# Kernel tuning notes

Measured on AMD Instinct MI355X. Metric: run time of the kernel, lower is better.

The kernel has to match this reference:

```python
import jax, jax.numpy as jnp
import numpy as np

S, D, H, L, FF = 4096, 128, 4, 3, 1024
DH = D // H
LN_EPS = 1e-5


def _layernorm(x, g, b):
    m = jnp.mean(x, axis=-1, keepdims=True)
    v = jnp.mean((x - m) ** 2, axis=-1, keepdims=True)
    return (x - m) * jax.lax.rsqrt(v + LN_EPS) * g + b


def setup_inputs() -> dict:
    key = jax.random.key(0)
    ks = jax.random.split(key, 16)
    w = lambda k, shp, s=0.05: jax.random.normal(k, shp, dtype=jnp.float32) * s
    return {
        "src": jax.random.normal(ks[0], (S, 1, D), dtype=jnp.float32),
        # per-layer transformer params, stacked on leading L axis
        "Wqkv": w(ks[1], (L, 3 * D, D)),
        "bqkv": jnp.zeros((L, 3 * D), jnp.float32),
        "Wo": w(ks[2], (L, D, D)),
        "bo": jnp.zeros((L, D), jnp.float32),
        "ln1_g": jnp.ones((L, D), jnp.float32),
        "ln1_b": jnp.zeros((L, D), jnp.float32),
        "W1": w(ks[3], (L, FF, D)),
        "b1": jnp.zeros((L, FF), jnp.float32),
        "W2": w(ks[4], (L, D, FF)),
        "b2": jnp.zeros((L, D), jnp.float32),
        "ln2_g": jnp.ones((L, D), jnp.float32),
        "ln2_b": jnp.zeros((L, D), jnp.float32),
        "fc1_W": w(ks[5], (D, D)),
        "fc1_b": jnp.zeros((D,), jnp.float32),
        "fc2_W": w(ks[6], (D, D)),
        "fc2_b": jnp.zeros((D,), jnp.float32),
    }


def reference(src, Wqkv, bqkv, Wo, bo, ln1_g, ln1_b, W1, b1, W2, b2,
              ln2_g, ln2_b, fc1_W, fc1_b, fc2_W, fc2_b):
    x = src[:, 0, :]  # [S, D] (batch=1, squeezed as in the torch module)
    scale = 1.0 / np.sqrt(DH).astype(np.float32)
    for l in range(L):  # small fixed layer count
        # --- self-attention (post-norm, as in torch TransformerEncoderLayer, eval mode) ---
        qkv = x @ Wqkv[l].T + bqkv[l]                      # [S, 3D]
        q, k, v = jnp.split(qkv, 3, axis=-1)
        q = q.reshape(S, H, DH)
        k = k.reshape(S, H, DH)
        v = v.reshape(S, H, DH)
        att = jax.nn.softmax(jnp.einsum('shd,thd->hst', q, k) * scale, axis=-1)
        o = jnp.einsum('hst,thd->shd', att, v).reshape(S, D)
        o = o @ Wo[l].T + bo[l]
        x = _layernorm(x + o, ln1_g[l], ln1_b[l])
        # --- feed-forward ---
        f = jax.nn.relu(x @ W1[l].T + b1[l]) @ W2[l].T + b2[l]
        x = _layernorm(x + f, ln2_g[l], ln2_b[l])
    # head
    x = jax.nn.relu(x @ fc1_W.T + fc1_b)
    x = x @ fc2_W.T + fc2_b
    # pairwise cosine similarity, clamped at min 1e-6 (vectorized form of pCosineSim)
    xn = x / jnp.linalg.norm(x, axis=1, keepdims=True)
    return jnp.maximum(xn @ xn.T, 1e-6)
```

## Files before the change

kernel.cpp:

```cpp
#include <hip/hip_runtime.h>
#include <math.h>

#define S 4096
#define QK_SCALE 0.17677669529663687f
#define LOG2E    1.44269504088896f
#define SPLIT 8
#define KS (S / SPLIT)

typedef _Float16 f16x8 __attribute__((ext_vector_type(8)));
typedef _Float16 f16x4 __attribute__((ext_vector_type(4)));
typedef _Float16 f16x2 __attribute__((ext_vector_type(2)));
typedef float f32x4 __attribute__((ext_vector_type(4)));


template<int ROWS>
__device__ __forceinline__ void stageGL(_Float16 (*dst)[128], const _Float16* src,
                                        int ld, int row0, int col0, int tid) {
    int w = tid >> 6, l = tid & 63;
    constexpr int NISS = ROWS / 16;
#pragma unroll
    for (int v = 0; v < NISS; v++) {
        int G = (w * NISS + v) * 64 + l;
        int row = G >> 4, g = G & 15;
        int gs = g ^ (row & 15);
        const void* gp = src + (size_t)(row0 + row) * ld + col0 + gs * 8;
        void* lp = (char*)&dst[0][0] + (size_t)G * 16;
        __builtin_amdgcn_global_load_lds(
            (const __attribute__((address_space(1))) void*)gp,
            (__attribute__((address_space(3))) void*)lp, 16, 0, 0);
    }
}

__device__ __forceinline__ f16x8 rdS(const _Float16 (*B)[128], int row, int qg) {
    return *(const f16x8*)&B[row][(qg ^ (row & 15)) << 3];
}
__device__ __forceinline__ void wrS(_Float16 (*B)[128], int row, int col, _Float16 v) {
    B[row][((((col >> 3) ^ (row & 15))) << 3) | (col & 7)] = v;
}

__global__ __launch_bounds__(256) void setup_cvt(const float* __restrict__ q,
                                                 const float* __restrict__ wo,
                                                 const float* __restrict__ w1,
                                                 const float* __restrict__ w2,
                                                 const float* __restrict__ f1,
                                                 const float* __restrict__ f2,
                                                 _Float16* __restrict__ dst,
                                                 const float* __restrict__ a,
                                                 float* __restrict__ x,
                                                 _Float16* __restrict__ xh)
{
    int bb = blockIdx.x;
    if (bb < 992) {
        const float* src; size_t dof; int lb;
        if (bb < 144)      { src = q;  dof = 0;      lb = bb; }
        else if (bb < 192) { src = wo; dof = 147456; lb = bb - 144; }
        else if (bb < 576) { src = w1; dof = 196608; lb = bb - 192; }
        else if (bb < 960) { src = w2; dof = 589824; lb = bb - 576; }
        else if (bb < 976) { src = f1; dof = 983040; lb = bb - 960; }
        else               { src = f2; dof = 999424; lb = bb - 976; }
        int i = lb * 1024 + threadIdx.x * 4;
        float4 v = *(const float4*)(src + i);
        f16x4 h = {(_Float16)v.x, (_Float16)v.y, (_Float16)v.z, (_Float16)v.w};
        *(f16x4*)(dst + dof + i) = h;
    } else {
        int i = (bb - 992) * 256 + threadIdx.x;
        float4 v = ((const float4*)a)[i];
        ((float4*)x)[i] = v;
        f16x4 h = {(_Float16)v.x, (_Float16)v.y, (_Float16)v.z, (_Float16)v.w};
        ((f16x4*)xh)[i] = h;
    }
}

__global__ __launch_bounds__(256) void gemm_qkv(const _Float16* __restrict__ xh,
                                                const _Float16* __restrict__ Wh,
                                                const float* __restrict__ bias,
                                                _Float16* __restrict__ qh,
                                                _Float16* __restrict__ kh,
                                                _Float16* __restrict__ vt)
{
    __shared__ _Float16 Ah[16][128], Bh[128][128];
    int tid = threadIdx.x, w = tid >> 6, l = tid & 63, lc = l & 15, lr = l >> 4;
    int m0 = blockIdx.x * 16, by = blockIdx.y;

    stageGL<16>(Ah, xh, 128, m0, 0, tid);
    stageGL<128>(Bh, Wh, 128, by * 128, 0, tid);
    __syncthreads();

    f32x4 acc[2];
#pragma unroll
    for (int j = 0; j < 2; j++) acc[j] = {0.f, 0.f, 0.f, 0.f};
#pragma unroll
    for (int ks = 0; ks < 4; ks++) {
        f16x8 af = rdS(Ah, lc, ks * 4 + lr);
#pragma unroll
        for (int j = 0; j < 2; j++) {
            f16x8 bf = rdS(Bh, w * 32 + j * 16 + lc, ks * 4 + lr);
            acc[j] = __builtin_amdgcn_mfma_f32_16x16x32_f16(af, bf, acc[j], 0, 0, 0);
        }
    }

    int mb = m0 + lr * 4;
#pragma unroll
    for (int j = 0; j < 2; j++) {
        int n = w * 32 + j * 16 + lc;
        float bb = bias[by * 128 + n];
        if (by == 0) {
#pragma unroll
            for (int r = 0; r < 4; r++)
                qh[(size_t)(mb + r) * 128 + n] =
                    (_Float16)((acc[j][r] + bb) * (QK_SCALE * LOG2E));
        } else if (by == 1) {
            int hh = n >> 5, d = n & 31;
#pragma unroll
            for (int r = 0; r < 4; r++)
                kh[((size_t)hh * S + mb + r) * 32 + d] = (_Float16)(acc[j][r] + bb);
        } else {
            f16x4 pk;
#pragma unroll
            for (int r = 0; r < 4; r++) pk[r] = (_Float16)(acc[j][r] + bb);
            *(f16x4*)&vt[(size_t)n * S + mb] = pk;
        }
    }
}

__global__ __launch_bounds__(256) void attn_mfma(const _Float16* __restrict__ qh,
                                                 const _Float16* __restrict__ kh,
                                                 const _Float16* __restrict__ vt,
                                                 _Float16* __restrict__ part,
                                                 float* __restrict__ mll)
{
    __shared__ _Float16 Ks[2][64][32];
    __shared__ _Float16 Vt[2][32][72];
    __shared__ _Float16 Ps[4][16][72];
    int h = blockIdx.y, q0 = blockIdx.x * 64, z = blockIdx.z;
    int tid = threadIdx.x;
    int w = tid >> 6, l = tid & 63;
    int lc = l & 15, lr = l >> 4;

    f16x8 qf = *(const f16x8*)&qh[(size_t)(q0 + w * 16 + lc) * 128 + h * 32 + lr * 8];

    const _Float16* khh = kh + (size_t)h * S * 32;
    const _Float16* vth = vt + (size_t)h * 32 * S;

    int krow = tid >> 2, kcol = (tid & 3) * 8;
    int vrow = tid >> 3, vcol = (tid & 7) * 8;

    f32x4 o0 = {0.f, 0.f, 0.f, 0.f}, o1 = {0.f, 0.f, 0.f, 0.f};
    float lp = 0.f;

    int k0 = z * KS;
    {
        f16x8 kr = *(const f16x8*)&khh[(size_t)(k0 + krow) * 32 + kcol];
        f16x8 vr = *(const f16x8*)&vth[(size_t)vrow * S + k0 + vcol];
        *(f16x8*)&Ks[0][krow][kcol] = kr;
        *(f16x8*)&Vt[0][vrow][vcol] = vr;
    }
    __syncthreads();

    int cur = 0;
#pragma unroll 1
    for (int t8 = 0; t8 < KS / 64; t8++) {
        bool more = (t8 + 1 < KS / 64);
        f16x8 kr, vr;
        if (more) {
            int kn = k0 + (t8 + 1) * 64;
            kr = *(const f16x8*)&khh[(size_t)(kn + krow) * 32 + kcol];
            vr = *(const f16x8*)&vth[(size_t)vrow * S + kn + vcol];
        }

        f32x4 st[4];
#pragma unroll
        for (int t = 0; t < 4; t++) {
            f16x8 kf = *(const f16x8*)&Ks[cur][t * 16 + lc][lr * 8];
            f32x4 zz = {0.f, 0.f, 0.f, 0.f};
            st[t] = __builtin_amdgcn_mfma_f32_16x16x32_f16(kf, qf, zz, 0, 0, 0);
        }
#pragma unroll
        for (int t = 0; t < 4; t++) {
            float p0 = exp2f(st[t][0]), p1 = exp2f(st[t][1]);
            float p2 = exp2f(st[t][2]), p3 = exp2f(st[t][3]);
            lp += (p0 + p1) + (p2 + p3);
            f16x2 h0 = {(_Float16)p0, (_Float16)p1};
            f16x2 h1 = {(_Float16)p2, (_Float16)p3};
            *(f16x2*)&Ps[w][lc][t * 16 + lr * 4]     = h0;
            *(f16x2*)&Ps[w][lc][t * 16 + lr * 4 + 2] = h1;
        }
        asm volatile("s_waitcnt lgkmcnt(0)" ::: "memory");
#pragma unroll
        for (int ch = 0; ch < 2; ch++) {
            f16x8 pf = *(const f16x8*)&Ps[w][lc][ch * 32 + lr * 8];
            f16x8 v0 = *(const f16x8*)&Vt[cur][lc][ch * 32 + lr * 8];
            f16x8 v1 = *(const f16x8*)&Vt[cur][16 + lc][ch * 32 + lr * 8];
            o0 = __builtin_amdgcn_mfma_f32_16x16x32_f16(pf, v0, o0, 0, 0, 0);
            o1 = __builtin_amdgcn_mfma_f32_16x16x32_f16(pf, v1, o1, 0, 0, 0);
        }
        if (more) {
            *(f16x8*)&Ks[cur ^ 1][krow][kcol] = kr;
            *(f16x8*)&Vt[cur ^ 1][vrow][vcol] = vr;
            __syncthreads();
        }
        cur ^= 1;
    }

    lp += __shfl_xor(lp, 16);
    lp += __shfl_xor(lp, 32);

    _Float16* pz = part + (size_t)z * 524288;
#pragma unroll
    for (int i = 0; i < 4; i++) {
        int q = q0 + w * 16 + lr * 4 + i;
        pz[(size_t)q * 128 + h * 32 + lc]      = (_Float16)o0[i];
        pz[(size_t)q * 128 + h * 32 + 16 + lc] = (_Float16)o1[i];
    }
    if (l < 16) mll[((size_t)z * 4 + h) * 4096 + q0 + w * 16 + lc] = lp;
}

__global__ __launch_bounds__(256) void wo_ln_merge(const _Float16* __restrict__ part,
                                                   const float* __restrict__ mll,
                                                   const _Float16* __restrict__ Wh,
                                                   const float* __restrict__ bias,
                                                   float* __restrict__ x,
                                                   _Float16* __restrict__ xh,
                                                   const float* __restrict__ g,
                                                   const float* __restrict__ b)
{
    __shared__ _Float16 Ah[16][128], Bh[128][128];
    __shared__ float Red[16][4][2];
    int tid = threadIdx.x, w = tid >> 6, l = tid & 63, lc = l & 15, lr = l >> 4;
    int m0 = blockIdx.x * 16;

    stageGL<128>(Bh, Wh, 128, 0, 0, tid);
    {
        int row = tid >> 4, qg = tid & 15;
        int col0 = qg * 8;
        int q = m0 + row, hh = col0 >> 5;
        float lsum = 0.f;
#pragma unroll
        for (int s = 0; s < SPLIT; s++) lsum += mll[((size_t)s * 4 + hh) * 4096 + q];
        float am[8];
#pragma unroll
        for (int e = 0; e < 8; e++) am[e] = 0.f;
#pragma unroll
        for (int s = 0; s < SPLIT; s++) {
            f16x8 t = *(const f16x8*)&part[(size_t)s * 524288 + (size_t)q * 128 + col0];
#pragma unroll
            for (int e = 0; e < 8; e++) am[e] += (float)t[e];
        }
        float inv = 1.f / lsum;
        f16x8 hv;
#pragma unroll
        for (int e = 0; e < 8; e++) hv[e] = (_Float16)(am[e] * inv);
        *(f16x8*)&Ah[row][(qg ^ (row & 15)) << 3] = hv;
    }
    __syncthreads();

    f32x4 acc[2];
#pragma unroll
    for (int j = 0; j < 2; j++) acc[j] = {0.f, 0.f, 0.f, 0.f};
#pragma unroll
    for (int ks = 0; ks < 4; ks++) {
        f16x8 af = rdS(Ah, lc, ks * 4 + lr);
#pragma unroll
        for (int j = 0; j < 2; j++) {
            f16x8 bf = rdS(Bh, w * 32 + j * 16 + lc, ks * 4 + lr);
            acc[j] = __builtin_amdgcn_mfma_f32_16x16x32_f16(af, bf, acc[j], 0, 0, 0);
        }
    }

#pragma unroll
    for (int j = 0; j < 2; j++) {
        int n = w * 32 + j * 16 + lc;
        float bb = bias[n];
#pragma unroll
        for (int r = 0; r < 4; r++)
            acc[j][r] += bb + x[(size_t)(m0 + lr * 4 + r) * 128 + n];
    }
#pragma unroll
    for (int r = 0; r < 4; r++) {
        float s1 = acc[0][r] + acc[1][r];
        float s2 = acc[0][r] * acc[0][r] + acc[1][r] * acc[1][r];
#pragma unroll
        for (int off = 1; off < 16; off <<= 1) {
            s1 += __shfl_xor(s1, off);
            s2 += __shfl_xor(s2, off);
        }
        if (lc == 0) { Red[lr * 4 + r][w][0] = s1; Red[lr * 4 + r][w][1] = s2; }
    }
    __syncthreads();
#pragma unroll
    for (int r = 0; r < 4; r++) {
        int rl = lr * 4 + r;
        float S1 = (Red[rl][0][0] + Red[rl][1][0]) + (Red[rl][2][0] + Red[rl][3][0]);
        float S2 = (Red[rl][0][1] + Red[rl][1][1]) + (Red[rl][2][1] + Red[rl][3][1]);
        float mean = S1 * (1.0f / 128.0f);
        float var = S2 * (1.0f / 128.0f) - mean * mean;
        float inv = rsqrtf(var + 1e-5f);
        int m = m0 + rl;
#pragma unroll
        for (int j = 0; j < 2; j++) {
            int n = w * 32 + j * 16 + lc;
            float o = (acc[j][r] - mean) * inv * g[n] + b[n];
            x[(size_t)m * 128 + n] = o;
            xh[(size_t)m * 128 + n] = (_Float16)o;
        }
    }
}

__global__ __launch_bounds__(256) void ffn_pair(const _Float16* __restrict__ xh,
                                                const _Float16* __restrict__ W1h,
                                                const float* __restrict__ b1,
                                                const _Float16* __restrict__ W2h,
                                                _Float16* __restrict__ wpart)
{
    __shared__ _Float16 Ah[64][128], Bh[128][128];
    int tid = threadIdx.x, w = tid >> 6, l = tid & 63, lc = l & 15, lr = l >> 4;
    int wr = w >> 1, wc = w & 1;
    int m0 = blockIdx.x * 64, c = blockIdx.y;

    stageGL<64>(Ah, xh, 128, m0, 0, tid);
    stageGL<128>(Bh, W1h, 128, c * 128, 0, tid);
    __syncthreads();

    f32x4 acc[2][4];
#pragma unroll
    for (int i = 0; i < 2; i++)
#pragma unroll
        for (int j = 0; j < 4; j++) acc[i][j] = {0.f, 0.f, 0.f, 0.f};
#pragma unroll
    for (int ks = 0; ks < 4; ks++) {
        f16x8 af0 = rdS(Ah, wr * 32 + lc, ks * 4 + lr);
        f16x8 af1 = rdS(Ah, wr * 32 + 16 + lc, ks * 4 + lr);
#pragma unroll
        for (int j = 0; j < 4; j++) {
            f16x8 bf = rdS(Bh, wc * 64 + j * 16 + lc, ks * 4 + lr);
            acc[0][j] = __builtin_amdgcn_mfma_f32_16x16x32_f16(af0, bf, acc[0][j], 0, 0, 0);
            acc[1][j] = __builtin_amdgcn_mfma_f32_16x16x32_f16(af1, bf, acc[1][j], 0, 0, 0);
        }
    }
    __syncthreads();

#pragma unroll
    for (int i = 0; i < 2; i++)
#pragma unroll
        for (int j = 0; j < 4; j++) {
            int n = wc * 64 + j * 16 + lc;
            float bb = b1[c * 128 + n];
#pragma unroll
            for (int r = 0; r < 4; r++)
                wrS(Ah, wr * 32 + i * 16 + lr * 4 + r, n,
                    (_Float16)fmaxf(acc[i][j][r] + bb, 0.f));
        }
    stageGL<128>(Bh, W2h, 1024, 0, c * 128, tid);
    __syncthreads();

    f32x4 oacc[2][4];
#pragma unroll
    for (int i = 0; i < 2; i++)
#pragma unroll
        for (int j = 0; j < 4; j++) oacc[i][j] = {0.f, 0.f, 0.f, 0.f};
#pragma unroll
    for (int ks = 0; ks < 4; ks++) {
        f16x8 af0 = rdS(Ah, wr * 32 + lc, ks * 4 + lr);
        f16x8 af1 = rdS(Ah, wr * 32 + 16 + lc, ks * 4 + lr);
#pragma unroll
        for (int j = 0; j < 4; j++) {
            f16x8 bf = rdS(Bh, wc * 64 + j * 16 + lc, ks * 4 + lr);
            oacc[0][j] = __builtin_amdgcn_mfma_f32_16x16x32_f16(af0, bf, oacc[0][j], 0, 0, 0);
            oacc[1][j] = __builtin_amdgcn_mfma_f32_16x16x32_f16(af1, bf, oacc[1][j], 0, 0, 0);
        }
    }

    _Float16* pz = wpart + (size_t)c * 524288;
#pragma unroll
    for (int i = 0; i < 2; i++) {
        int mb = m0 + wr * 32 + i * 16 + lr * 4;
#pragma unroll
        for (int j = 0; j < 4; j++) {
            int n = wc * 64 + j * 16 + lc;
#pragma unroll
            for (int r = 0; r < 4; r++)
                pz[(size_t)(mb + r) * 128 + n] = (_Float16)oacc[i][j][r];
        }
    }
}

__global__ __launch_bounds__(256) void reduce8_ln(const _Float16* __restrict__ part,
                                                  const float* __restrict__ bias,
                                                  float* __restrict__ x,
                                                  _Float16* __restrict__ xh,
                                                  const float* __restrict__ g,
                                                  const float* __restrict__ b)
{
    int row  = blockIdx.x * 4 + (threadIdx.x >> 6);
    int lane = threadIdx.x & 63;
    size_t base = (size_t)row * 128;
    int c = lane * 2;
    float a0 = 0.f, a1 = 0.f;
#pragma unroll
    for (int s = 0; s < 8; s++) {
        f16x2 p = *(const f16x2*)&part[(size_t)s * 524288 + base + c];
        a0 += (float)p[0]; a1 += (float)p[1];
    }
    float2 bv = *(const float2*)&bias[c];
    float2 xv = *(const float2*)&x[base + c];
    a0 += bv.x + xv.x; a1 += bv.y + xv.y;
    float s = a0 + a1;
#pragma unroll
    for (int off = 32; off; off >>= 1) s += __shfl_xor(s, off);
    float mean = s * (1.0f / 128.0f);
    float d0 = a0 - mean, d1 = a1 - mean;
    float v = d0 * d0 + d1 * d1;
#pragma unroll
    for (int off = 32; off; off >>= 1) v += __shfl_xor(v, off);
    float inv = rsqrtf(v * (1.0f / 128.0f) + 1e-5f);
    float2 gv = *(const float2*)&g[c];
    float2 bb = *(const float2*)&b[c];
    float o0 = d0 * inv * gv.x + bb.x, o1 = d1 * inv * gv.y + bb.y;
    float2 r; r.x = o0; r.y = o1;
    *(float2*)&x[base + c] = r;
    f16x2 rh = {(_Float16)o0, (_Float16)o1};
    *(f16x2*)&xh[base + c] = rh;
}

__global__ __launch_bounds__(256) void fc_fused(const _Float16* __restrict__ xh,
                                                const _Float16* __restrict__ W1h,
                                                const float* __restrict__ b1f,
                                                const _Float16* __restrict__ W2h,
                                                const float* __restrict__ b2f,
                                                _Float16* __restrict__ aoh)
{
    __shared__ _Float16 Ah[16][128], Bh[128][128];
    __shared__ float Red[16][4];
    int tid = threadIdx.x, w = tid >> 6, l = tid & 63, lc = l & 15, lr = l >> 4;
    int m0 = blockIdx.x * 16;

    stageGL<16>(Ah, xh, 128, m0, 0, tid);
    stageGL<128>(Bh, W1h, 128, 0, 0, tid);
    __syncthreads();

    f32x4 acc[2];
#pragma unroll
    for (int j = 0; j < 2; j++) acc[j] = {0.f, 0.f, 0.f, 0.f};
#pragma unroll
    for (int ks = 0; ks < 4; ks++) {
        f16x8 af = rdS(Ah, lc, ks * 4 + lr);
#pragma unroll
        for (int j = 0; j < 2; j++) {
            f16x8 bf = rdS(Bh, w * 32 + j * 16 + lc, ks * 4 + lr);
            acc[j] = __builtin_amdgcn_mfma_f32_16x16x32_f16(af, bf, acc[j], 0, 0, 0);
        }
    }
    __syncthreads();
#pragma unroll
    for (int j = 0; j < 2; j++) {
        int n = w * 32 + j * 16 + lc;
        float bb = b1f[n];
#pragma unroll
        for (int r = 0; r < 4; r++)
            wrS(Ah, lr * 4 + r, n, (_Float16)fmaxf(acc[j][r] + bb, 0.f));
    }
    stageGL<128>(Bh, W2h, 128, 0, 0, tid);
    __syncthreads();

    f32x4 o[2];
#pragma unroll
    for (int j = 0; j < 2; j++) o[j] = {0.f, 0.f, 0.f, 0.f};
#pragma unroll
    for (int ks = 0; ks < 4; ks++) {
        f16x8 af = rdS(Ah, lc, ks * 4 + lr);
#pragma unroll
        for (int j = 0; j < 2; j++) {
            f16x8 bf = rdS(Bh, w * 32 + j * 16 + lc, ks * 4 + lr);
            o[j] = __builtin_amdgcn_mfma_f32_16x16x32_f16(af, bf, o[j], 0, 0, 0);
        }
    }
#pragma unroll
    for (int j = 0; j < 2; j++) {
        float bb = b2f[w * 32 + j * 16 + lc];
#pragma unroll
        for (int r = 0; r < 4; r++) o[j][r] += bb;
    }
#pragma unroll
    for (int r = 0; r < 4; r++) {
        float s2 = o[0][r] * o[0][r] + o[1][r] * o[1][r];
#pragma unroll
        for (int off = 1; off < 16; off <<= 1) s2 += __shfl_xor(s2, off);
        if (lc == 0) Red[lr * 4 + r][w] = s2;
    }
    __syncthreads();
#pragma unroll
    for (int r = 0; r < 4; r++) {
        int rl = lr * 4 + r;
        float inv = rsqrtf((Red[rl][0] + Red[rl][1]) + (Red[rl][2] + Red[rl][3]));
        int m = m0 + rl;
#pragma unroll
        for (int j = 0; j < 2; j++) {
            int n = w * 32 + j * 16 + lc;
            aoh[(size_t)m * 128 + n] = (_Float16)(o[j][r] * inv);
        }
    }
}

__global__ __launch_bounds__(256) void gram_f16(const _Float16* __restrict__ aoh,
                                                float* __restrict__ C)
{
    __shared__ _Float16 Ah[64][128], Bh[128][128];
    int tid = threadIdx.x, w = tid >> 6, l = tid & 63, lc = l & 15, lr = l >> 4;
    int wr = w >> 1, wc = w & 1;
    int m0 = blockIdx.x * 64, n0 = blockIdx.y * 128;

    stageGL<64>(Ah, aoh, 128, m0, 0, tid);
    stageGL<128>(Bh, aoh, 128, n0, 0, tid);
    __syncthreads();

    f32x4 acc[2][4];
#pragma unroll
    for (int i = 0; i < 2; i++)
#pragma unroll
        for (int j = 0; j < 4; j++) acc[i][j] = {0.f, 0.f, 0.f, 0.f};
#pragma unroll
    for (int ks = 0; ks < 4; ks++) {
        f16x8 af0 = rdS(Ah, wr * 32 + lc, ks * 4 + lr);
        f16x8 af1 = rdS(Ah, wr * 32 + 16 + lc, ks * 4 + lr);
#pragma unroll
        for (int j = 0; j < 4; j++) {
            f16x8 bf = rdS(Bh, wc * 64 + j * 16 + lc, ks * 4 + lr);
            acc[0][j] = __builtin_amdgcn_mfma_f32_16x16x32_f16(af0, bf, acc[0][j], 0, 0, 0);
            acc[1][j] = __builtin_amdgcn_mfma_f32_16x16x32_f16(af1, bf, acc[1][j], 0, 0, 0);
        }
    }

#pragma unroll
    for (int i = 0; i < 2; i++) {
        int mb = m0 + wr * 32 + i * 16 + lr * 4;
#pragma unroll
        for (int j = 0; j < 4; j++) {
            int n = n0 + wc * 64 + j * 16 + lc;
#pragma unroll
            for (int r = 0; r < 4; r++)
                C[(size_t)(mb + r) * 4096 + n] = fmaxf(acc[i][j][r], 1e-6f);
        }
    }
}

extern "C" void kernel_launch(void* const* d_in, const int* in_sizes, int n_in,
                              void* d_out, int out_size, void* d_ws, size_t ws_size,
                              hipStream_t stream)
{
    const float* src  = (const float*)d_in[0];
    const float* Wqkv = (const float*)d_in[1];
    const float* bqkv = (const float*)d_in[2];
    const float* Wo   = (const float*)d_in[3];
    const float* bo   = (const float*)d_in[4];
    const float* ln1g = (const float*)d_in[5];
    const float* ln1b = (const float*)d_in[6];
    const float* W1   = (const float*)d_in[7];
    const float* b1   = (const float*)d_in[8];
    const float* W2   = (const float*)d_in[9];
    const float* b2   = (const float*)d_in[10];
    const float* ln2g = (const float*)d_in[11];
    const float* ln2b = (const float*)d_in[12];
    const float* fc1W = (const float*)d_in[13];
    const float* fc1b = (const float*)d_in[14];
    const float* fc2W = (const float*)d_in[15];
    const float* fc2b = (const float*)d_in[16];

    float* ws = (float*)d_ws;
    float*    x   = ws;
    _Float16* xh  = (_Float16*)(ws + 524288);
    _Float16* aoh = (_Float16*)(ws + 786432);
    _Float16* qh  = (_Float16*)(ws + 1048576);
    _Float16* kh  = (_Float16*)(ws + 1310720);
    _Float16* vt  = (_Float16*)(ws + 1572864);
    float*    mll = ws + 1835008;

    _Float16* wpart = (_Float16*)d_out + 4194304;
    _Float16* apart = (_Float16*)d_out + 12582912;
    _Float16* wh    = (_Float16*)d_out + 16777216;
    float*    out   = (float*)d_out;

    _Float16* qkvh = wh;
    _Float16* woh  = wh + 147456;
    _Float16* w1h  = wh + 196608;
    _Float16* w2h  = wh + 589824;
    _Float16* fc1h = wh + 983040;
    _Float16* fc2h = wh + 999424;

    setup_cvt<<<1504, 256, 0, stream>>>(Wqkv, Wo, W1, W2, fc1W, fc2W, wh,
                                        src, x, xh);
    for (int l = 0; l < 3; l++) {
        gemm_qkv<<<dim3(256, 3), 256, 0, stream>>>(xh, qkvh + l * 49152,
                                                   bqkv + l * 384, qh, kh, vt);
        attn_mfma<<<dim3(64, 4, SPLIT), 256, 0, stream>>>(qh, kh, vt, apart, mll);
        wo_ln_merge<<<256, 256, 0, stream>>>(apart, mll, woh + l * 16384, bo + l * 128,
                                             x, xh, ln1g + l * 128, ln1b + l * 128);
        ffn_pair<<<dim3(64, 8), 256, 0, stream>>>(xh, w1h + l * 131072, b1 + l * 1024,
                                                  w2h + l * 131072, wpart);
        reduce8_ln<<<1024, 256, 0, stream>>>(wpart, b2 + l * 128, x, xh,
                                             ln2g + l * 128, ln2b + l * 128);
    }
    fc_fused<<<256, 256, 0, stream>>>(xh, fc1h, fc1b, fc2h, fc2b, aoh);
    gram_f16<<<dim3(64, 32), 256, 0, stream>>>(aoh, out);
}
```

Measured before the change: 264.0 us.

## Fuse FFN split-K reduction and LayerNorm into next QKV GEMM and head

```diff
diff --git a/kernel.cpp b/kernel.cpp
--- a/kernel.cpp
+++ b/kernel.cpp
@@ -123,6 +123,99 @@
     }
 }
 
+__global__ __launch_bounds__(256) void gemm_qkv_merge(
+    const _Float16* __restrict__ wpart, const float* __restrict__ x1,
+    const float* __restrict__ b2, const float* __restrict__ g2,
+    const float* __restrict__ bn2, float* __restrict__ x0,
+    const _Float16* __restrict__ Wh, const float* __restrict__ bias,
+    _Float16* __restrict__ qh, _Float16* __restrict__ kh,
+    _Float16* __restrict__ vt)
+{
+    __shared__ _Float16 Ah[16][128], Bh[128][128];
+    int tid = threadIdx.x, w = tid >> 6, l = tid & 63, lc = l & 15, lr = l >> 4;
+    int m0 = blockIdx.x * 16, by = blockIdx.y;
+
+    stageGL<128>(Bh, Wh, 128, by * 128, 0, tid);
+    {
+        int row = tid >> 4, qg = tid & 15, col0 = qg * 8;
+        int q = m0 + row;
+        float am[8];
+#pragma unroll
+        for (int e = 0; e < 8; e++) am[e] = 0.f;
+#pragma unroll
+        for (int s = 0; s < 8; s++) {
+            f16x8 t = *(const f16x8*)&wpart[(size_t)s * 524288 + (size_t)q * 128 + col0];
+#pragma unroll
+            for (int e = 0; e < 8; e++) am[e] += (float)t[e];
+        }
+#pragma unroll
+        for (int e = 0; e < 8; e++)
+            am[e] += b2[col0 + e] + x1[(size_t)q * 128 + col0 + e];
+        float s1 = 0.f, s2 = 0.f;
+#pragma unroll
+        for (int e = 0; e < 8; e++) { s1 += am[e]; s2 += am[e] * am[e]; }
+#pragma unroll
+        for (int off = 1; off < 16; off <<= 1) {
+            s1 += __shfl_xor(s1, off);
+            s2 += __shfl_xor(s2, off);
+        }
+        float mean = s1 * (1.0f / 128.0f);
+        float var = s2 * (1.0f / 128.0f) - mean * mean;
+        float inv = rsqrtf(var + 1e-5f);
+        float o[8];
+        f16x8 hv;
+#pragma unroll
+        for (int e = 0; e < 8; e++) {
+            o[e] = (am[e] - mean) * inv * g2[col0 + e] + bn2[col0 + e];
+            hv[e] = (_Float16)o[e];
+        }
+        *(f16x8*)&Ah[row][(qg ^ (row & 15)) << 3] = hv;
+        if (by == 0) {
+            float4 v0 = {o[0], o[1], o[2], o[3]};
+            float4 v1 = {o[4], o[5], o[6], o[7]};
+            *(float4*)&x0[(size_t)q * 128 + col0]     = v0;
+            *(float4*)&x0[(size_t)q * 128 + col0 + 4] = v1;
+        }
+    }
+    __syncthreads();
+
+    f32x4 acc[2];
+#pragma unroll
+    for (int j = 0; j < 2; j++) acc[j] = {0.f, 0.f, 0.f, 0.f};
+#pragma unroll
+    for (int ks = 0; ks < 4; ks++) {
+        f16x8 af = rdS(Ah, lc, ks * 4 + lr);
+#pragma unroll
+        for (int j = 0; j < 2; j++) {
+            f16x8 bf = rdS(Bh, w * 32 + j * 16 + lc, ks * 4 + lr);
+            acc[j] = __builtin_amdgcn_mfma_f32_16x16x32_f16(af, bf, acc[j], 0, 0, 0);
+        }
+    }
+
+    int mb = m0 + lr * 4;
+#pragma unroll
+    for (int j = 0; j < 2; j++) {
+        int n = w * 32 + j * 16 + lc;
+        float bb = bias[by * 128 + n];
+        if (by == 0) {
+#pragma unroll
+            for (int r = 0; r < 4; r++)
+                qh[(size_t)(mb + r) * 128 + n] =
+                    (_Float16)((acc[j][r] + bb) * (QK_SCALE * LOG2E));
+        } else if (by == 1) {
+            int hh = n >> 5, d = n & 31;
+#pragma unroll
+            for (int r = 0; r < 4; r++)
+                kh[((size_t)hh * S + mb + r) * 32 + d] = (_Float16)(acc[j][r] + bb);
+        } else {
+            f16x4 pk;
+#pragma unroll
+            for (int r = 0; r < 4; r++) pk[r] = (_Float16)(acc[j][r] + bb);
+            *(f16x4*)&vt[(size_t)n * S + mb] = pk;
+        }
+    }
+}
+
 __global__ __launch_bounds__(256) void attn_mfma(const _Float16* __restrict__ qh,
                                                  const _Float16* __restrict__ kh,
                                                  const _Float16* __restrict__ vt,
@@ -219,7 +312,8 @@
                                                    const float* __restrict__ mll,
                                                    const _Float16* __restrict__ Wh,
                                                    const float* __restrict__ bias,
-                                                   float* __restrict__ x,
+                                                   const float* __restrict__ xres,
+                                                   float* __restrict__ xo,
                                                    _Float16* __restrict__ xh,
                                                    const float* __restrict__ g,
                                                    const float* __restrict__ b)
@@ -273,7 +367,7 @@
         float bb = bias[n];
 #pragma unroll
         for (int r = 0; r < 4; r++)
-            acc[j][r] += bb + x[(size_t)(m0 + lr * 4 + r) * 128 + n];
+            acc[j][r] += bb + xres[(size_t)(m0 + lr * 4 + r) * 128 + n];
     }
 #pragma unroll
     for (int r = 0; r < 4; r++) {
@@ -300,7 +394,7 @@
         for (int j = 0; j < 2; j++) {
             int n = w * 32 + j * 16 + lc;
             float o = (acc[j][r] - mean) * inv * g[n] + b[n];
-            x[(size_t)m * 128 + n] = o;
+            xo[(size_t)m * 128 + n] = o;
             xh[(size_t)m * 128 + n] = (_Float16)o;
         }
     }
@@ -384,45 +478,11 @@
     }
 }
 
-__global__ __launch_bounds__(256) void reduce8_ln(const _Float16* __restrict__ part,
-                                                  const float* __restrict__ bias,
-                                                  float* __restrict__ x,
-                                                  _Float16* __restrict__ xh,
-                                                  const float* __restrict__ g,
-                                                  const float* __restrict__ b)
-{
-    int row  = blockIdx.x * 4 + (threadIdx.x >> 6);
-    int lane = threadIdx.x & 63;
-    size_t base = (size_t)row * 128;
-    int c = lane * 2;
-    float a0 = 0.f, a1 = 0.f;
-#pragma unroll
-    for (int s = 0; s < 8; s++) {
-        f16x2 p = *(const f16x2*)&part[(size_t)s * 524288 + base + c];
-        a0 += (float)p[0]; a1 += (float)p[1];
-    }
-    float2 bv = *(const float2*)&bias[c];
-    float2 xv = *(const float2*)&x[base + c];
-    a0 += bv.x + xv.x; a1 += bv.y + xv.y;
-    float s = a0 + a1;
-#pragma unroll
-    for (int off = 32; off; off >>= 1) s += __shfl_xor(s, off);
-    float mean = s * (1.0f / 128.0f);
-    float d0 = a0 - mean, d1 = a1 - mean;
-    float v = d0 * d0 + d1 * d1;
-#pragma unroll
-    for (int off = 32; off; off >>= 1) v += __shfl_xor(v, off);
-    float inv = rsqrtf(v * (1.0f / 128.0f) + 1e-5f);
-    float2 gv = *(const float2*)&g[c];
-    float2 bb = *(const float2*)&b[c];
-    float o0 = d0 * inv * gv.x + bb.x, o1 = d1 * inv * gv.y + bb.y;
-    float2 r; r.x = o0; r.y = o1;
-    *(float2*)&x[base + c] = r;
-    f16x2 rh = {(_Float16)o0, (_Float16)o1};
-    *(f16x2*)&xh[base + c] = rh;
-}
-
-__global__ __launch_bounds__(256) void fc_fused(const _Float16* __restrict__ xh,
+__global__ __launch_bounds__(256) void fc_fused(const _Float16* __restrict__ wpart,
+                                                const float* __restrict__ x1,
+                                                const float* __restrict__ b2l,
+                                                const float* __restrict__ g2,
+                                                const float* __restrict__ bn2,
                                                 const _Float16* __restrict__ W1h,
                                                 const float* __restrict__ b1f,
                                                 const _Float16* __restrict__ W2h,
@@ -434,8 +494,39 @@
     int tid = threadIdx.x, w = tid >> 6, l = tid & 63, lc = l & 15, lr = l >> 4;
     int m0 = blockIdx.x * 16;
 
-    stageGL<16>(Ah, xh, 128, m0, 0, tid);
     stageGL<128>(Bh, W1h, 128, 0, 0, tid);
+    {
+        int row = tid >> 4, qg = tid & 15, col0 = qg * 8;
+        int q = m0 + row;
+        float am[8];
+#pragma unroll
+        for (int e = 0; e < 8; e++) am[e] = 0.f;
+#pragma unroll
+        for (int s = 0; s < 8; s++) {
+            f16x8 t = *(const f16x8*)&wpart[(size_t)s * 524288 + (size_t)q * 128 + col0];
+#pragma unroll
+            for (int e = 0; e < 8; e++) am[e] += (float)t[e];
+        }
+#pragma unroll
+        for (int e = 0; e < 8; e++)
+            am[e] += b2l[col0 + e] + x1[(size_t)q * 128 + col0 + e];
+        float s1 = 0.f, s2 = 0.f;
+#pragma unroll
+        for (int e = 0; e < 8; e++) { s1 += am[e]; s2 += am[e] * am[e]; }
+#pragma unroll
+        for (int off = 1; off < 16; off <<= 1) {
+            s1 += __shfl_xor(s1, off);
+            s2 += __shfl_xor(s2, off);
+        }
+        float mean = s1 * (1.0f / 128.0f);
+        float var = s2 * (1.0f / 128.0f) - mean * mean;
+        float inv = rsqrtf(var + 1e-5f);
+        f16x8 hv;
+#pragma unroll
+        for (int e = 0; e < 8; e++)
+            hv[e] = (_Float16)((am[e] - mean) * inv * g2[col0 + e] + bn2[col0 + e]);
+        *(f16x8*)&Ah[row][(qg ^ (row & 15)) << 3] = hv;
+    }
     __syncthreads();
 
     f32x4 acc[2];
@@ -577,6 +668,7 @@
     _Float16* wpart = (_Float16*)d_out + 4194304;
     _Float16* apart = (_Float16*)d_out + 12582912;
     _Float16* wh    = (_Float16*)d_out + 16777216;
+    float*    x1    = (float*)d_out + 9437184;
     float*    out   = (float*)d_out;
 
     _Float16* qkvh = wh;
@@ -588,17 +680,25 @@
 
     setup_cvt<<<1504, 256, 0, stream>>>(Wqkv, Wo, W1, W2, fc1W, fc2W, wh,
                                         src, x, xh);
-    for (int l = 0; l < 3; l++) {
-        gemm_qkv<<<dim3(256, 3), 256, 0, stream>>>(xh, qkvh + l * 49152,
-                                                   bqkv + l * 384, qh, kh, vt);
+    gemm_qkv<<<dim3(256, 3), 256, 0, stream>>>(xh, qkvh, bqkv, qh, kh, vt);
+    attn_mfma<<<dim3(64, 4, SPLIT), 256, 0, stream>>>(qh, kh, vt, apart, mll);
+    wo_ln_merge<<<256, 256, 0, stream>>>(apart, mll, woh, bo, x, x1, xh,
+                                         ln1g, ln1b);
+    ffn_pair<<<dim3(64, 8), 256, 0, stream>>>(xh, w1h, b1, w2h, wpart);
+    for (int l = 1; l < 3; l++) {
+        gemm_qkv_merge<<<dim3(256, 3), 256, 0, stream>>>(
+            wpart, x1, b2 + (l - 1) * 128, ln2g + (l - 1) * 128,
+            ln2b + (l - 1) * 128, x,
+            qkvh + l * 49152, bqkv + l * 384, qh, kh, vt);
         attn_mfma<<<dim3(64, 4, SPLIT), 256, 0, stream>>>(qh, kh, vt, apart, mll);
-        wo_ln_merge<<<256, 256, 0, stream>>>(apart, mll, woh + l * 16384, bo + l * 128,
-                                             x, xh, ln1g + l * 128, ln1b + l * 128);
-        ffn_pair<<<dim3(64, 8), 256, 0, stream>>>(xh, w1h + l * 131072, b1 + l * 1024,
+        wo_ln_merge<<<256, 256, 0, stream>>>(apart, mll, woh + l * 16384,
+                                             bo + l * 128, x, x1, xh,
+                                             ln1g + l * 128, ln1b + l * 128);
+        ffn_pair<<<dim3(64, 8), 256, 0, stream>>>(xh, w1h + l * 131072,
+                                                  b1 + l * 1024,
                                                   w2h + l * 131072, wpart);
-        reduce8_ln<<<1024, 256, 0, stream>>>(wpart, b2 + l * 128, x, xh,
-                                             ln2g + l * 128, ln2b + l * 128);
-    }
-    fc_fused<<<256, 256, 0, stream>>>(xh, fc1h, fc1b, fc2h, fc2b, aoh);
+    }
+    fc_fused<<<256, 256, 0, stream>>>(wpart, x1, b2 + 256, ln2g + 256,
+                                      ln2b + 256, fc1h, fc1b, fc2h, fc2b, aoh);
     gram_f16<<<dim3(64, 32), 256, 0, stream>>>(aoh, out);
 }
```

Result: no change. 260.9 us (-1.2%).
